# Performance work log

Measured on AMD Instinct MI355X. Metric: run time of the kernel, lower is better.

Reference implementation:

```python
import jax, jax.numpy as jnp
import numpy as np

N = 100000      # user + item nodes
E = 600000      # number of edges
LATDIM = 128
HEAD = 4
HDIM = LATDIM // HEAD


def setup_inputs() -> dict:
    key = jax.random.key(0)
    ks = jax.random.split(key, 7)
    return {
        "embeds": jax.random.normal(ks[0], (N, LATDIM), dtype=jnp.float32),
        "qTrans": jax.random.normal(ks[1], (LATDIM, LATDIM), dtype=jnp.float32) * (1.0 / np.sqrt(LATDIM)),
        "kTrans": jax.random.normal(ks[2], (LATDIM, LATDIM), dtype=jnp.float32) * (1.0 / np.sqrt(LATDIM)),
        "vTrans": jax.random.normal(ks[3], (LATDIM, LATDIM), dtype=jnp.float32) * (1.0 / np.sqrt(LATDIM)),
        "filt": jax.random.normal(ks[4], (N, HEAD), dtype=jnp.float32),
        "rows": jax.random.randint(ks[5], (E,), 0, N, dtype=jnp.int32),
        "cols": jax.random.randint(ks[6], (E,), 0, N, dtype=jnp.int32),
    }


def reference(embeds, qTrans, kTrans, vTrans, filt, rows, cols):
    # gather endpoint embeddings: [E, latdim]
    rowEmbeds = embeds[rows]
    colEmbeds = embeds[cols]
    # per-edge multi-head q/k/v: [E, H, D]
    qEmbeds = (rowEmbeds @ qTrans).reshape(E, HEAD, HDIM)
    kEmbeds = (colEmbeds @ kTrans).reshape(E, HEAD, HDIM)
    vEmbeds = (colEmbeds @ vTrans).reshape(E, HEAD, HDIM)
    # per-edge per-head attention logits
    att = jnp.einsum('ehd,ehd->eh', qEmbeds, kEmbeds)
    att = jnp.clip(att, -10.0, 10.0)
    att = att + filt[cols]
    expAtt = jnp.exp(att)
    # segment softmax over destination rows
    attNorm = jax.ops.segment_sum(expAtt, rows, num_segments=N)[rows]
    att = expAtt / (attNorm + 1e-8)
    # weighted values, scatter-sum back to nodes
    resEdges = (att[:, :, None] * vEmbeds).reshape(E, LATDIM)
    resEmbeds = jax.ops.segment_sum(resEdges, rows, num_segments=N)
    return resEmbeds
```

## Files before the change

### kernel.cpp

```cpp
#include <hip/hip_runtime.h>

#define N_NODES 100000
#define E_EDGES 600000
#define LATDIM 128
#define HEAD 4
#define HDIM 32

#define SCAN_CHUNK 1024
#define SCAN_NB ((N_NODES + SCAN_CHUNK - 1) / SCAN_CHUNK)

typedef __bf16 bf16x8 __attribute__((ext_vector_type(8)));
typedef float  f32x4  __attribute__((ext_vector_type(4)));

__device__ __forceinline__ unsigned f32_to_bf16_rne(float x) {
    unsigned u = __float_as_uint(x);
    u += 0x7fffu + ((u >> 16) & 1u);
    return u >> 16;
}

__device__ __forceinline__ void bf16_split(float x, unsigned& hi, unsigned& lo) {
    unsigned hb = f32_to_bf16_rne(x);
    float hf = __uint_as_float(hb << 16);
    unsigned lb = f32_to_bf16_rne(x - hf);
    hi = hb; lo = lb;
}

__global__ __launch_bounds__(256) void wprep_kernel(
    const float* __restrict__ qT, const float* __restrict__ kT,
    const float* __restrict__ vT,
    unsigned short* __restrict__ WThi, unsigned short* __restrict__ WTlo)
{
    int g = blockIdx.x * 256 + threadIdx.x;
    if (g >= 3072) return;
    int m    = g >> 10;
    int rem  = g & 1023;
    int c    = rem >> 3;
    int k0   = (rem & 7) * 16;
    const float* W = (m == 0) ? qT : (m == 1) ? kT : vT;

    unsigned short hi[16], lo[16];
    #pragma unroll
    for (int j = 0; j < 16; ++j) {
        float x = W[(size_t)(k0 + j) * 128 + c];
        unsigned hb, lb;
        bf16_split(x, hb, lb);
        hi[j] = (unsigned short)hb;
        lo[j] = (unsigned short)lb;
    }
    size_t off = (size_t)m * 16384 + (size_t)c * 128 + k0;
    *(uint4*)(WThi + off)     = *(const uint4*)&hi[0];
    *(uint4*)(WThi + off + 8) = *(const uint4*)&hi[8];
    *(uint4*)(WTlo + off)     = *(const uint4*)&lo[0];
    *(uint4*)(WTlo + off + 8) = *(const uint4*)&lo[8];
}

__global__ __launch_bounds__(256, 2) void qkv_mfma_kernel(
    const float* __restrict__ embeds,
    const unsigned short* __restrict__ WThi,
    const unsigned short* __restrict__ WTlo,
    float* __restrict__ Q, unsigned* __restrict__ KV)
{
    __shared__ __align__(16) char smem[65536];
    char* Ahi = smem;
    char* Alo = smem + 16384;
    char* Bhi = smem + 32768;
    char* Blo = smem + 49152;

    const int tid = threadIdx.x;
    const int rowBase = blockIdx.x * 64;

    #pragma unroll
    for (int it = 0; it < 8; ++it) {
        int idx = it * 256 + tid;
        int r  = idx >> 5;
        int c4 = idx & 31;
        int gr = rowBase + r;
        float4 v = make_float4(0.f, 0.f, 0.f, 0.f);
        if (gr < N_NODES) v = ((const float4*)embeds)[(size_t)gr * 32 + c4];
        unsigned hx, lx, hy, ly, hz, lz, hw, lw;
        bf16_split(v.x, hx, lx); bf16_split(v.y, hy, ly);
        bf16_split(v.z, hz, lz); bf16_split(v.w, hw, lw);
        uint2 hp = make_uint2(hx | (hy << 16), hz | (hw << 16));
        uint2 lp = make_uint2(lx | (ly << 16), lz | (lw << 16));
        int byte = r * 256 + c4 * 8;
        int swz  = byte ^ ((r & 7) << 4);
        *(uint2*)(Ahi + swz) = hp;
        *(uint2*)(Alo + swz) = lp;
    }
    __syncthreads();

    const int lane = tid & 63;
    const int wv   = tid >> 6;
    const int lrow = lane & 15;
    const int kg   = lane >> 4;
    const int arow = wv * 16 + lrow;

    bf16x8 a_hi[4], a_lo[4];
    #pragma unroll
    for (int kk = 0; kk < 4; ++kk) {
        int byte = arow * 256 + kk * 64 + kg * 16;
        int swz  = byte ^ ((lrow & 7) << 4);
        a_hi[kk] = __builtin_bit_cast(bf16x8, *(const uint4*)(Ahi + swz));
        a_lo[kk] = __builtin_bit_cast(bf16x8, *(const uint4*)(Alo + swz));
    }

    const int orow = kg << 2;

    for (int h = 0; h < 2; ++h) {
        f32x4 kreg[4];
        for (int m = 0; m < 3; ++m) {
            __syncthreads();
            {
                const char* srch = (const char*)(WThi + (size_t)m * 16384 + (size_t)h * 8192);
                const char* srcl = (const char*)(WTlo + (size_t)m * 16384 + (size_t)h * 8192);
                #pragma unroll
                for (int it = 0; it < 4; ++it) {
                    int idx  = it * 256 + tid;
                    int cl   = idx >> 4;
                    int byte = idx * 16;
                    int swz  = (cl * 256 + (idx & 15) * 16) ^ ((cl & 7) << 4);
                    *(uint4*)(Bhi + swz) = *(const uint4*)(srch + byte);
                    *(uint4*)(Blo + swz) = *(const uint4*)(srcl + byte);
                }
            }
            __syncthreads();

            f32x4 acc[4] = { {0.f,0.f,0.f,0.f}, {0.f,0.f,0.f,0.f},
                             {0.f,0.f,0.f,0.f}, {0.f,0.f,0.f,0.f} };
            #pragma unroll
            for (int kk = 0; kk < 4; ++kk) {
                #pragma unroll
                for (int n = 0; n < 4; ++n) {
                    int brow = n * 16 + lrow;
                    int byte = brow * 256 + kk * 64 + kg * 16;
                    int swz  = byte ^ ((lrow & 7) << 4);
                    bf16x8 bh = __builtin_bit_cast(bf16x8, *(const uint4*)(Bhi + swz));
                    bf16x8 bl = __builtin_bit_cast(bf16x8, *(const uint4*)(Blo + swz));
                    acc[n] = __builtin_amdgcn_mfma_f32_16x16x32_bf16(a_hi[kk], bh, acc[n], 0, 0, 0);
                    acc[n] = __builtin_amdgcn_mfma_f32_16x16x32_bf16(a_lo[kk], bh, acc[n], 0, 0, 0);
                    acc[n] = __builtin_amdgcn_mfma_f32_16x16x32_bf16(a_hi[kk], bl, acc[n], 0, 0, 0);
                }
            }

            if (m == 0) {
                #pragma unroll
                for (int n = 0; n < 4; ++n)
                    #pragma unroll
                    for (int j = 0; j < 4; ++j) {
                        int gr  = rowBase + wv * 16 + orow + j;
                        int col = h * 64 + n * 16 + lrow;
                        if (gr < N_NODES) Q[(size_t)gr * 128 + col] = acc[n][j];
                    }
            } else if (m == 1) {
                #pragma unroll
                for (int n = 0; n < 4; ++n) kreg[n] = acc[n];
            } else {
                #pragma unroll
                for (int n = 0; n < 4; ++n)
                    #pragma unroll
                    for (int j = 0; j < 4; ++j) {
                        int gr  = rowBase + wv * 16 + orow + j;
                        int col = h * 64 + n * 16 + lrow;
                        if (gr < N_NODES) {
                            unsigned p = f32_to_bf16_rne(kreg[n][j])
                                       | (f32_to_bf16_rne(acc[n][j]) << 16);
                            KV[(size_t)gr * 128 + col] = p;
                        }
                    }
            }
        }
    }
}

__global__ __launch_bounds__(256) void hist_kernel(
    const int* __restrict__ rows, int* __restrict__ counts)
{
    int e = blockIdx.x * 256 + threadIdx.x;
    if (e < E_EDGES) atomicAdd(&counts[rows[e]], 1);
}

__global__ __launch_bounds__(256) void scan1_kernel(
    const int* __restrict__ counts, int* __restrict__ starts,
    int* __restrict__ blockSums)
{
    __shared__ int s[256];
    int b = blockIdx.x, t = threadIdx.x;
    int base = b * SCAN_CHUNK + t * 4;
    int v0 = (base + 0 < N_NODES) ? counts[base + 0] : 0;
    int v1 = (base + 1 < N_NODES) ? counts[base + 1] : 0;
    int v2 = (base + 2 < N_NODES) ? counts[base + 2] : 0;
    int v3 = (base + 3 < N_NODES) ? counts[base + 3] : 0;
    int local = v0 + v1 + v2 + v3;
    s[t] = local;
    __syncthreads();
    for (int off = 1; off < 256; off <<= 1) {
        int x = (t >= off) ? s[t - off] : 0;
        __syncthreads();
        s[t] += x;
        __syncthreads();
    }
    int incl = s[t];
    int excl = incl - local;
    if (base + 0 < N_NODES) starts[base + 0] = excl;
    if (base + 1 < N_NODES) starts[base + 1] = excl + v0;
    if (base + 2 < N_NODES) starts[base + 2] = excl + v0 + v1;
    if (base + 3 < N_NODES) starts[base + 3] = excl + v0 + v1 + v2;
    if (t == 255) blockSums[b] = incl;
}

__global__ __launch_bounds__(128) void scan2_kernel(int* __restrict__ blockSums)
{
    __shared__ int s[128];
    int t = threadIdx.x;
    int v = (t < SCAN_NB) ? blockSums[t] : 0;
    s[t] = v;
    __syncthreads();
    for (int off = 1; off < 128; off <<= 1) {
        int x = (t >= off) ? s[t - off] : 0;
        __syncthreads();
        s[t] += x;
        __syncthreads();
    }
    if (t < SCAN_NB) blockSums[t] = s[t] - v;
}

__global__ __launch_bounds__(256) void scan3_kernel(
    int* __restrict__ starts, const int* __restrict__ blockSums,
    int* __restrict__ cursor)
{
    int i = blockIdx.x * 256 + threadIdx.x;
    if (i < N_NODES) {
        int v = starts[i] + blockSums[i >> 10];
        starts[i] = v;
        cursor[i] = v;
    }
}

__global__ __launch_bounds__(256) void scatter_kernel(
    const int* __restrict__ rows, const int* __restrict__ cols,
    int* __restrict__ cursor, int* __restrict__ csrCols)
{
    int e = blockIdx.x * 256 + threadIdx.x;
    if (e >= E_EDGES) return;
    int pos = atomicAdd(&cursor[rows[e]], 1);
    csrCols[pos] = cols[e];
}

__global__ __launch_bounds__(256) void att_agg_kernel(
    const float* __restrict__ Q, const unsigned* __restrict__ KV,
    const float* __restrict__ filt,
    const int* __restrict__ starts, const int* __restrict__ counts,
    const int* __restrict__ csrCols,
    float* __restrict__ out)
{
    int t = threadIdx.x;
    int node = blockIdx.x * 8 + (t >> 5);
    if (node >= N_NODES) return;
    int lane = t & 31;
    int h = lane >> 3;

    float4 q = ((const float4*)(Q + (size_t)node * 128))[lane];
    int s   = starts[node];
    int cnt = counts[node];

    float norm = 0.f;
    float ax = 0.f, ay = 0.f, az = 0.f, aw = 0.f;

    int i = 0;
    for (; i + 2 <= cnt; i += 2) {
        int c0 = csrCols[s + i];
        int c1 = csrCols[s + i + 1];
        uint4 kv0 = ((const uint4*)KV)[(size_t)c0 * 32 + lane];
        uint4 kv1 = ((const uint4*)KV)[(size_t)c1 * 32 + lane];
        float f0 = filt[c0 * HEAD + h];
        float f1 = filt[c1 * HEAD + h];

        float k0x = __uint_as_float(kv0.x << 16), v0x = __uint_as_float(kv0.x & 0xffff0000u);
        float k0y = __uint_as_float(kv0.y << 16), v0y = __uint_as_float(kv0.y & 0xffff0000u);
        float k0z = __uint_as_float(kv0.z << 16), v0z = __uint_as_float(kv0.z & 0xffff0000u);
        float k0w = __uint_as_float(kv0.w << 16), v0w = __uint_as_float(kv0.w & 0xffff0000u);
        float k1x = __uint_as_float(kv1.x << 16), v1x = __uint_as_float(kv1.x & 0xffff0000u);
        float k1y = __uint_as_float(kv1.y << 16), v1y = __uint_as_float(kv1.y & 0xffff0000u);
        float k1z = __uint_as_float(kv1.z << 16), v1z = __uint_as_float(kv1.z & 0xffff0000u);
        float k1w = __uint_as_float(kv1.w << 16), v1w = __uint_as_float(kv1.w & 0xffff0000u);

        float p0 = q.x * k0x + q.y * k0y + q.z * k0z + q.w * k0w;
        float p1 = q.x * k1x + q.y * k1y + q.z * k1z + q.w * k1w;
        p0 += __shfl_xor(p0, 1);   p1 += __shfl_xor(p1, 1);
        p0 += __shfl_xor(p0, 2);   p1 += __shfl_xor(p1, 2);
        p0 += __shfl_xor(p0, 4);   p1 += __shfl_xor(p1, 4);

        float w0 = __expf(fminf(fmaxf(p0, -10.f), 10.f) + f0);
        float w1 = __expf(fminf(fmaxf(p1, -10.f), 10.f) + f1);
        norm += w0 + w1;
        ax += w0 * v0x + w1 * v1x;
        ay += w0 * v0y + w1 * v1y;
        az += w0 * v0z + w1 * v1z;
        aw += w0 * v0w + w1 * v1w;
    }
    if (i < cnt) {
        int c0 = csrCols[s + i];
        uint4 kv0 = ((const uint4*)KV)[(size_t)c0 * 32 + lane];
        float f0 = filt[c0 * HEAD + h];
        float k0x = __uint_as_float(kv0.x << 16), v0x = __uint_as_float(kv0.x & 0xffff0000u);
        float k0y = __uint_as_float(kv0.y << 16), v0y = __uint_as_float(kv0.y & 0xffff0000u);
        float k0z = __uint_as_float(kv0.z << 16), v0z = __uint_as_float(kv0.z & 0xffff0000u);
        float k0w = __uint_as_float(kv0.w << 16), v0w = __uint_as_float(kv0.w & 0xffff0000u);
        float p0 = q.x * k0x + q.y * k0y + q.z * k0z + q.w * k0w;
        p0 += __shfl_xor(p0, 1);
        p0 += __shfl_xor(p0, 2);
        p0 += __shfl_xor(p0, 4);
        float w0 = __expf(fminf(fmaxf(p0, -10.f), 10.f) + f0);
        norm += w0;
        ax += w0 * v0x; ay += w0 * v0y; az += w0 * v0z; aw += w0 * v0w;
    }
    float inv = 1.0f / (norm + 1e-8f);
    ((float4*)(out + (size_t)node * 128))[lane] =
        make_float4(ax * inv, ay * inv, az * inv, aw * inv);
}

extern "C" void kernel_launch(void* const* d_in, const int* in_sizes, int n_in,
                              void* d_out, int out_size, void* d_ws, size_t ws_size,
                              hipStream_t stream) {
    const float* embeds = (const float*)d_in[0];
    const float* qT     = (const float*)d_in[1];
    const float* kT     = (const float*)d_in[2];
    const float* vT     = (const float*)d_in[3];
    const float* filt   = (const float*)d_in[4];
    const int*   rows   = (const int*)d_in[5];
    const int*   cols   = (const int*)d_in[6];
    float*       out    = (float*)d_out;

    float*    Q  = (float*)d_ws;
    unsigned* KV = (unsigned*)(Q + (size_t)N_NODES * 128);
    int* counts    = (int*)(KV + (size_t)N_NODES * 128);
    int* starts    = counts + N_NODES;
    int* cursor    = starts + N_NODES;
    int* blockSums = cursor + N_NODES;
    int* csrCols   = blockSums + 128;

    unsigned short* WThi = (unsigned short*)csrCols;
    unsigned short* WTlo = WThi + 3 * 128 * 128;

    hipMemsetAsync(counts, 0, sizeof(int) * N_NODES, stream);

    wprep_kernel<<<12, 256, 0, stream>>>(qT, kT, vT, WThi, WTlo);
    qkv_mfma_kernel<<<(N_NODES + 63) / 64, 256, 0, stream>>>(embeds, WThi, WTlo, Q, KV);

    hist_kernel<<<(E_EDGES + 255) / 256, 256, 0, stream>>>(rows, counts);
    scan1_kernel<<<SCAN_NB, 256, 0, stream>>>(counts, starts, blockSums);
    scan2_kernel<<<1, 128, 0, stream>>>(blockSums);
    scan3_kernel<<<(N_NODES + 255) / 256, 256, 0, stream>>>(starts, blockSums, cursor);
    scatter_kernel<<<(E_EDGES + 255) / 256, 256, 0, stream>>>(rows, cols, cursor, csrCols);

    att_agg_kernel<<<(N_NODES + 7) / 8, 256, 0, stream>>>(
        Q, KV, filt, starts, counts, csrCols, out);
}
```

Measured before the change: 291.2 us.

## Prefetch next weight tile into registers during MFMA in QKV projection kernel

```diff
diff --git a/kernel.cpp b/kernel.cpp
--- a/kernel.cpp
+++ b/kernel.cpp
@@ -68,6 +68,18 @@
 
     const int tid = threadIdx.x;
     const int rowBase = blockIdx.x * 64;
+
+    uint4 pbh[4], pbl[4];
+    {
+        const char* srch = (const char*)WThi;
+        const char* srcl = (const char*)WTlo;
+        #pragma unroll
+        for (int it = 0; it < 4; ++it) {
+            int idx = it * 256 + tid;
+            pbh[it] = *(const uint4*)(srch + idx * 16);
+            pbl[it] = *(const uint4*)(srcl + idx * 16);
+        }
+    }
 
     #pragma unroll
     for (int it = 0; it < 8; ++it) {
@@ -95,6 +107,15 @@
     const int kg   = lane >> 4;
     const int arow = wv * 16 + lrow;
 
+    #pragma unroll
+    for (int it = 0; it < 4; ++it) {
+        int idx  = it * 256 + tid;
+        int cl   = idx >> 4;
+        int swz  = (cl * 256 + (idx & 15) * 16) ^ ((cl & 7) << 4);
+        *(uint4*)(Bhi + swz) = pbh[it];
+        *(uint4*)(Blo + swz) = pbl[it];
+    }
+
     bf16x8 a_hi[4], a_lo[4];
     #pragma unroll
     for (int kk = 0; kk < 4; ++kk) {
@@ -103,71 +124,84 @@
         a_hi[kk] = __builtin_bit_cast(bf16x8, *(const uint4*)(Ahi + swz));
         a_lo[kk] = __builtin_bit_cast(bf16x8, *(const uint4*)(Alo + swz));
     }
+    __syncthreads();
 
     const int orow = kg << 2;
 
-    for (int h = 0; h < 2; ++h) {
-        f32x4 kreg[4];
-        for (int m = 0; m < 3; ++m) {
+    f32x4 kreg[4];
+
+    #pragma unroll
+    for (int p = 0; p < 6; ++p) {
+        const int h = p / 3;
+        const int m = p % 3;
+
+        if (p < 5) {
+            const int hn = (p + 1) / 3, mn = (p + 1) % 3;
+            const char* srch = (const char*)(WThi + (size_t)mn * 16384 + (size_t)hn * 8192);
+            const char* srcl = (const char*)(WTlo + (size_t)mn * 16384 + (size_t)hn * 8192);
+            #pragma unroll
+            for (int it = 0; it < 4; ++it) {
+                int idx = it * 256 + tid;
+                pbh[it] = *(const uint4*)(srch + idx * 16);
+                pbl[it] = *(const uint4*)(srcl + idx * 16);
+            }
+        }
+
+        f32x4 acc[4] = { {0.f,0.f,0.f,0.f}, {0.f,0.f,0.f,0.f},
+                         {0.f,0.f,0.f,0.f}, {0.f,0.f,0.f,0.f} };
+        #pragma unroll
+        for (int kk = 0; kk < 4; ++kk) {
+            #pragma unroll
+            for (int n = 0; n < 4; ++n) {
+                int brow = n * 16 + lrow;
+                int byte = brow * 256 + kk * 64 + kg * 16;
+                int swz  = byte ^ ((lrow & 7) << 4);
+                bf16x8 bh = __builtin_bit_cast(bf16x8, *(const uint4*)(Bhi + swz));
+                bf16x8 bl = __builtin_bit_cast(bf16x8, *(const uint4*)(Blo + swz));
+                acc[n] = __builtin_amdgcn_mfma_f32_16x16x32_bf16(a_hi[kk], bh, acc[n], 0, 0, 0);
+                acc[n] = __builtin_amdgcn_mfma_f32_16x16x32_bf16(a_lo[kk], bh, acc[n], 0, 0, 0);
+                acc[n] = __builtin_amdgcn_mfma_f32_16x16x32_bf16(a_hi[kk], bl, acc[n], 0, 0, 0);
+            }
+        }
+
+        if (m == 0) {
+            #pragma unroll
+            for (int n = 0; n < 4; ++n)
+                #pragma unroll
+                for (int j = 0; j < 4; ++j) {
+                    int gr  = rowBase + wv * 16 + orow + j;
+                    int col = h * 64 + n * 16 + lrow;
+                    if (gr < N_NODES) Q[(size_t)gr * 128 + col] = acc[n][j];
+                }
+        } else if (m == 1) {
+            #pragma unroll
+            for (int n = 0; n < 4; ++n) kreg[n] = acc[n];
+        } else {
+            #pragma unroll
+            for (int n = 0; n < 4; ++n)
+                #pragma unroll
+                for (int j = 0; j < 4; ++j) {
+                    int gr  = rowBase + wv * 16 + orow + j;
+                    int col = h * 64 + n * 16 + lrow;
+                    if (gr < N_NODES) {
+                        unsigned pk = f32_to_bf16_rne(kreg[n][j])
+                                    | (f32_to_bf16_rne(acc[n][j]) << 16);
+                        KV[(size_t)gr * 128 + col] = pk;
+                    }
+                }
+        }
+
+        if (p < 5) {
             __syncthreads();
-            {
-                const char* srch = (const char*)(WThi + (size_t)m * 16384 + (size_t)h * 8192);
-                const char* srcl = (const char*)(WTlo + (size_t)m * 16384 + (size_t)h * 8192);
-                #pragma unroll
-                for (int it = 0; it < 4; ++it) {
-                    int idx  = it * 256 + tid;
-                    int cl   = idx >> 4;
-                    int byte = idx * 16;
-                    int swz  = (cl * 256 + (idx & 15) * 16) ^ ((cl & 7) << 4);
-                    *(uint4*)(Bhi + swz) = *(const uint4*)(srch + byte);
-                    *(uint4*)(Blo + swz) = *(const uint4*)(srcl + byte);
-                }
+            #pragma unroll
+            for (int it = 0; it < 4; ++it) {
+                int idx  = it * 256 + tid;
+                int cl   = idx >> 4;
+                int swz  = (cl * 256 + (idx & 15) * 16) ^ ((cl & 7) << 4);
+                *(uint4*)(Bhi + swz) = pbh[it];
+                *(uint4*)(Blo + swz) = pbl[it];
             }
             __syncthreads();
-
-            f32x4 acc[4] = { {0.f,0.f,0.f,0.f}, {0.f,0.f,0.f,0.f},
-                             {0.f,0.f,0.f,0.f}, {0.f,0.f,0.f,0.f} };
-            #pragma unroll
-            for (int kk = 0; kk < 4; ++kk) {
-                #pragma unroll
-                for (int n = 0; n < 4; ++n) {
-                    int brow = n * 16 + lrow;
-                    int byte = brow * 256 + kk * 64 + kg * 16;
-                    int swz  = byte ^ ((lrow & 7) << 4);
-                    bf16x8 bh = __builtin_bit_cast(bf16x8, *(const uint4*)(Bhi + swz));
-                    bf16x8 bl = __builtin_bit_cast(bf16x8, *(const uint4*)(Blo + swz));
-                    acc[n] = __builtin_amdgcn_mfma_f32_16x16x32_bf16(a_hi[kk], bh, acc[n], 0, 0, 0);
-                    acc[n] = __builtin_amdgcn_mfma_f32_16x16x32_bf16(a_lo[kk], bh, acc[n], 0, 0, 0);
-                    acc[n] = __builtin_amdgcn_mfma_f32_16x16x32_bf16(a_hi[kk], bl, acc[n], 0, 0, 0);
-                }
-            }
-
-            if (m == 0) {
-                #pragma unroll
-                for (int n = 0; n < 4; ++n)
-                    #pragma unroll
-                    for (int j = 0; j < 4; ++j) {
-                        int gr  = rowBase + wv * 16 + orow + j;
-                        int col = h * 64 + n * 16 + lrow;
-                        if (gr < N_NODES) Q[(size_t)gr * 128 + col] = acc[n][j];
-                    }
-            } else if (m == 1) {
-                #pragma unroll
-                for (int n = 0; n < 4; ++n) kreg[n] = acc[n];
-            } else {
-                #pragma unroll
-                for (int n = 0; n < 4; ++n)
-                    #pragma unroll
-                    for (int j = 0; j < 4; ++j) {
-                        int gr  = rowBase + wv * 16 + orow + j;
-                        int col = h * 64 + n * 16 + lrow;
-                        if (gr < N_NODES) {
-                            unsigned p = f32_to_bf16_rne(kreg[n][j])
-                                       | (f32_to_bf16_rne(acc[n][j]) << 16);
-                            KV[(size_t)gr * 128 + col] = p;
-                        }
-                    }
-            }
         }
     }
 }
```

After: 342.9 us. 17.8% more time.

## Halve QKV kernel LDS and prefetch weight panels into registers

Applied to the files above, without the earlier changes.

```diff
diff --git a/kernel.cpp b/kernel.cpp
--- a/kernel.cpp
+++ b/kernel.cpp
@@ -54,20 +54,99 @@
     *(uint4*)(WTlo + off + 8) = *(const uint4*)&lo[8];
 }
 
-__global__ __launch_bounds__(256, 2) void qkv_mfma_kernel(
+__global__ __launch_bounds__(256, 4) void qkv_mfma_kernel(
     const float* __restrict__ embeds,
     const unsigned short* __restrict__ WThi,
     const unsigned short* __restrict__ WTlo,
     float* __restrict__ Q, unsigned* __restrict__ KV)
 {
-    __shared__ __align__(16) char smem[65536];
+    __shared__ __align__(16) char smem[32768];
     char* Ahi = smem;
     char* Alo = smem + 16384;
-    char* Bhi = smem + 32768;
-    char* Blo = smem + 49152;
+    char* Bhi = smem;
+    char* Blo = smem + 16384;
 
     const int tid = threadIdx.x;
     const int rowBase = blockIdx.x * 64;
+
+    uint4 pbh0, pbh1, pbh2, pbh3;
+    uint4 pbl0, pbl1, pbl2, pbl3;
+
+#define PF(MN, HN) do {                                                          \
+        const char* _sh = (const char*)(WThi + (size_t)(MN) * 16384 + (size_t)(HN) * 8192); \
+        const char* _sl = (const char*)(WTlo + (size_t)(MN) * 16384 + (size_t)(HN) * 8192); \
+        pbh0 = *(const uint4*)(_sh + (size_t)(0 * 256 + tid) * 16);              \
+        pbh1 = *(const uint4*)(_sh + (size_t)(1 * 256 + tid) * 16);              \
+        pbh2 = *(const uint4*)(_sh + (size_t)(2 * 256 + tid) * 16);              \
+        pbh3 = *(const uint4*)(_sh + (size_t)(3 * 256 + tid) * 16);              \
+        pbl0 = *(const uint4*)(_sl + (size_t)(0 * 256 + tid) * 16);              \
+        pbl1 = *(const uint4*)(_sl + (size_t)(1 * 256 + tid) * 16);              \
+        pbl2 = *(const uint4*)(_sl + (size_t)(2 * 256 + tid) * 16);              \
+        pbl3 = *(const uint4*)(_sl + (size_t)(3 * 256 + tid) * 16);              \
+    } while (0)
+
+#define COMMIT() do {                                                            \
+        { int _i = 0 * 256 + tid; int _c = _i >> 4;                              \
+          int _s = (_c * 256 + (_i & 15) * 16) ^ ((_c & 7) << 4);                \
+          *(uint4*)(Bhi + _s) = pbh0; *(uint4*)(Blo + _s) = pbl0; }              \
+        { int _i = 1 * 256 + tid; int _c = _i >> 4;                              \
+          int _s = (_c * 256 + (_i & 15) * 16) ^ ((_c & 7) << 4);                \
+          *(uint4*)(Bhi + _s) = pbh1; *(uint4*)(Blo + _s) = pbl1; }              \
+        { int _i = 2 * 256 + tid; int _c = _i >> 4;                              \
+          int _s = (_c * 256 + (_i & 15) * 16) ^ ((_c & 7) << 4);                \
+          *(uint4*)(Bhi + _s) = pbh2; *(uint4*)(Blo + _s) = pbl2; }              \
+        { int _i = 3 * 256 + tid; int _c = _i >> 4;                              \
+          int _s = (_c * 256 + (_i & 15) * 16) ^ ((_c & 7) << 4);                \
+          *(uint4*)(Bhi + _s) = pbh3; *(uint4*)(Blo + _s) = pbl3; }              \
+    } while (0)
+
+#define MFMA_PANEL(ACC) do {                                                     \
+        _Pragma("unroll")                                                        \
+        for (int kk = 0; kk < 4; ++kk) {                                         \
+            _Pragma("unroll")                                                    \
+            for (int n = 0; n < 4; ++n) {                                        \
+                int brow = n * 16 + lrow;                                        \
+                int byte = brow * 256 + kk * 64 + kg * 16;                       \
+                int swz  = byte ^ ((lrow & 7) << 4);                             \
+                bf16x8 bh = __builtin_bit_cast(bf16x8, *(const uint4*)(Bhi + swz)); \
+                bf16x8 bl = __builtin_bit_cast(bf16x8, *(const uint4*)(Blo + swz)); \
+                ACC[n] = __builtin_amdgcn_mfma_f32_16x16x32_bf16(a_hi[kk], bh, ACC[n], 0, 0, 0); \
+                ACC[n] = __builtin_amdgcn_mfma_f32_16x16x32_bf16(a_lo[kk], bh, ACC[n], 0, 0, 0); \
+                ACC[n] = __builtin_amdgcn_mfma_f32_16x16x32_bf16(a_hi[kk], bl, ACC[n], 0, 0, 0); \
+            }                                                                    \
+        }                                                                        \
+    } while (0)
+
+#define ZACC(ACC) f32x4 ACC[4] = { {0.f,0.f,0.f,0.f}, {0.f,0.f,0.f,0.f},         \
+                                   {0.f,0.f,0.f,0.f}, {0.f,0.f,0.f,0.f} }
+
+#define STORE_Q(ACC, H) do {                                                     \
+        _Pragma("unroll")                                                        \
+        for (int n = 0; n < 4; ++n)                                              \
+        _Pragma("unroll")                                                        \
+        for (int j = 0; j < 4; ++j) {                                            \
+            int gr  = rowBase + wv * 16 + orow + j;                              \
+            int col = (H) * 64 + n * 16 + lrow;                                  \
+            if (gr < N_NODES) Q[(size_t)gr * 128 + col] = ACC[n][j];             \
+        }                                                                        \
+    } while (0)
+
+#define STORE_KV(ACC, H) do {                                                    \
+        _Pragma("unroll")                                                        \
+        for (int n = 0; n < 4; ++n)                                              \
+        _Pragma("unroll")                                                        \
+        for (int j = 0; j < 4; ++j) {                                            \
+            int gr  = rowBase + wv * 16 + orow + j;                              \
+            int col = (H) * 64 + n * 16 + lrow;                                  \
+            if (gr < N_NODES) {                                                  \
+                unsigned pk = f32_to_bf16_rne(kreg[n][j])                        \
+                            | (f32_to_bf16_rne(ACC[n][j]) << 16);                \
+                KV[(size_t)gr * 128 + col] = pk;                                 \
+            }                                                                    \
+        }                                                                        \
+    } while (0)
+
+    PF(0, 0);
 
     #pragma unroll
     for (int it = 0; it < 8; ++it) {
@@ -94,6 +173,7 @@
     const int lrow = lane & 15;
     const int kg   = lane >> 4;
     const int arow = wv * 16 + lrow;
+    const int orow = kg << 2;
 
     bf16x8 a_hi[4], a_lo[4];
     #pragma unroll
@@ -103,73 +183,60 @@
         a_hi[kk] = __builtin_bit_cast(bf16x8, *(const uint4*)(Ahi + swz));
         a_lo[kk] = __builtin_bit_cast(bf16x8, *(const uint4*)(Alo + swz));
     }
-
-    const int orow = kg << 2;
-
-    for (int h = 0; h < 2; ++h) {
-        f32x4 kreg[4];
-        for (int m = 0; m < 3; ++m) {
-            __syncthreads();
-            {
-                const char* srch = (const char*)(WThi + (size_t)m * 16384 + (size_t)h * 8192);
-                const char* srcl = (const char*)(WTlo + (size_t)m * 16384 + (size_t)h * 8192);
-                #pragma unroll
-                for (int it = 0; it < 4; ++it) {
-                    int idx  = it * 256 + tid;
-                    int cl   = idx >> 4;
-                    int byte = idx * 16;
-                    int swz  = (cl * 256 + (idx & 15) * 16) ^ ((cl & 7) << 4);
-                    *(uint4*)(Bhi + swz) = *(const uint4*)(srch + byte);
-                    *(uint4*)(Blo + swz) = *(const uint4*)(srcl + byte);
-                }
-            }
-            __syncthreads();
-
-            f32x4 acc[4] = { {0.f,0.f,0.f,0.f}, {0.f,0.f,0.f,0.f},
-                             {0.f,0.f,0.f,0.f}, {0.f,0.f,0.f,0.f} };
-            #pragma unroll
-            for (int kk = 0; kk < 4; ++kk) {
-                #pragma unroll
-                for (int n = 0; n < 4; ++n) {
-                    int brow = n * 16 + lrow;
-                    int byte = brow * 256 + kk * 64 + kg * 16;
-                    int swz  = byte ^ ((lrow & 7) << 4);
-                    bf16x8 bh = __builtin_bit_cast(bf16x8, *(const uint4*)(Bhi + swz));
-                    bf16x8 bl = __builtin_bit_cast(bf16x8, *(const uint4*)(Blo + swz));
-                    acc[n] = __builtin_amdgcn_mfma_f32_16x16x32_bf16(a_hi[kk], bh, acc[n], 0, 0, 0);
-                    acc[n] = __builtin_amdgcn_mfma_f32_16x16x32_bf16(a_lo[kk], bh, acc[n], 0, 0, 0);
-                    acc[n] = __builtin_amdgcn_mfma_f32_16x16x32_bf16(a_hi[kk], bl, acc[n], 0, 0, 0);
-                }
-            }
-
-            if (m == 0) {
-                #pragma unroll
-                for (int n = 0; n < 4; ++n)
-                    #pragma unroll
-                    for (int j = 0; j < 4; ++j) {
-                        int gr  = rowBase + wv * 16 + orow + j;
-                        int col = h * 64 + n * 16 + lrow;
-                        if (gr < N_NODES) Q[(size_t)gr * 128 + col] = acc[n][j];
-                    }
-            } else if (m == 1) {
-                #pragma unroll
-                for (int n = 0; n < 4; ++n) kreg[n] = acc[n];
-            } else {
-                #pragma unroll
-                for (int n = 0; n < 4; ++n)
-                    #pragma unroll
-                    for (int j = 0; j < 4; ++j) {
-                        int gr  = rowBase + wv * 16 + orow + j;
-                        int col = h * 64 + n * 16 + lrow;
-                        if (gr < N_NODES) {
-                            unsigned p = f32_to_bf16_rne(kreg[n][j])
-                                       | (f32_to_bf16_rne(acc[n][j]) << 16);
-                            KV[(size_t)gr * 128 + col] = p;
-                        }
-                    }
-            }
-        }
-    }
+    __syncthreads();
+
+    COMMIT();
+    __syncthreads();
+
+    f32x4 kreg[4];
+
+    {
+        PF(1, 0);
+        ZACC(acc);
+        MFMA_PANEL(acc);
+        STORE_Q(acc, 0);
+        __syncthreads(); COMMIT(); __syncthreads();
+    }
+    {
+        PF(2, 0);
+        ZACC(acc);
+        MFMA_PANEL(acc);
+        kreg[0] = acc[0]; kreg[1] = acc[1]; kreg[2] = acc[2]; kreg[3] = acc[3];
+        __syncthreads(); COMMIT(); __syncthreads();
+    }
+    {
+        PF(0, 1);
+        ZACC(acc);
+        MFMA_PANEL(acc);
+        STORE_KV(acc, 0);
+        __syncthreads(); COMMIT(); __syncthreads();
+    }
+    {
+        PF(1, 1);
+        ZACC(acc);
+        MFMA_PANEL(acc);
+        STORE_Q(acc, 1);
+        __syncthreads(); COMMIT(); __syncthreads();
+    }
+    {
+        PF(2, 1);
+        ZACC(acc);
+        MFMA_PANEL(acc);
+        kreg[0] = acc[0]; kreg[1] = acc[1]; kreg[2] = acc[2]; kreg[3] = acc[3];
+        __syncthreads(); COMMIT(); __syncthreads();
+    }
+    {
+        ZACC(acc);
+        MFMA_PANEL(acc);
+        STORE_KV(acc, 1);
+    }
+
+#undef PF
+#undef COMMIT
+#undef MFMA_PANEL
+#undef ZACC
+#undef STORE_Q
+#undef STORE_KV
 }
 
 __global__ __launch_bounds__(256) void hist_kernel(
```

New measurement: 295.2 us. About the same (+1.4%).
